# Performance work log

Hardware: AMD Instinct MI355X
Metric: run time of the kernel (lower is better)

## Reference

```python
import jax, jax.numpy as jnp
import numpy as np

D_OUT, D1, D2 = 512, 512, 512
R0, R1, R2 = 128, 128, 128
BATCH = 8192


def setup_inputs() -> dict:
    key = jax.random.key(0)
    k1, k2, k3, k4, k5, k6 = jax.random.split(key, 6)
    return {
        "X1": jax.random.normal(k1, (D1, BATCH), dtype=jnp.float32),
        "X2": jax.random.normal(k2, (D2, BATCH), dtype=jnp.float32),
        "U0": jax.random.normal(k3, (D_OUT, R0), dtype=jnp.float32) * 0.05,
        "U1": jax.random.normal(k4, (D1, R1), dtype=jnp.float32) * 0.05,
        "U2": jax.random.normal(k5, (D2, R2), dtype=jnp.float32) * 0.05,
        "G": jax.random.normal(k6, (R0, R1, R2), dtype=jnp.float32) * 0.05,
    }


def reference(X1, X2, U0, U1, U2, G):
    # Per-mode projections: UX_i = U_{i+1}^T @ X_i  -> [r_i, B]
    UX1 = U1.T @ X1  # [R1, B]
    UX2 = U2.T @ X2  # [R2, B]
    # Column-wise Khatri-Rao product of UX1, UX2 gives kron per column with
    # row index q*R2 + r (C order), which matches mode-0 unfolding of G.
    # Fused form: core = G_(0) @ khatri_rao(UX1, UX2), expressed as one einsum.
    core = jnp.einsum('pqr,qb,rb->pb', G, UX1, UX2)  # [R0, B]
    Z = U0 @ core  # [D_OUT, B]
    return Z
```

## Files before the change

kernel.cpp:

```cpp
#include <hip/hip_runtime.h>
#include <hip/hip_bf16.h>
#include <stdint.h>


typedef __attribute__((ext_vector_type(8))) short bf8;
typedef __attribute__((ext_vector_type(4))) short bf4;
typedef __attribute__((ext_vector_type(4))) float f4;

__device__ __forceinline__ unsigned short f2bf(float f){
  unsigned x = __builtin_bit_cast(unsigned, f);
  x += 0x7fffu + ((x >> 16) & 1u);
  return (unsigned short)(x >> 16);
}
__device__ __forceinline__ float bf2f(unsigned short u){
  unsigned x = ((unsigned)u) << 16;
  return __builtin_bit_cast(float, x);
}
__device__ __forceinline__ void glds16(const void* g, void* l){
  __builtin_amdgcn_global_load_lds(
      (const __attribute__((address_space(1))) void*)g,
      (__attribute__((address_space(3))) void*)l, 16, 0, 0);
}

__global__ __launch_bounds__(256) void k_cast(const float* __restrict__ G,
                                              const float* __restrict__ U0,
                                              const float* __restrict__ U1,
                                              const float* __restrict__ U2,
                                              unsigned short* __restrict__ Gbf,
                                              unsigned short* __restrict__ U0bf,
                                              unsigned short* __restrict__ U1T,
                                              unsigned short* __restrict__ U2T){
  const int blk = blockIdx.x;
  if (blk < 2112){
    const int i4 = blk * 256 + threadIdx.x;
    const int NG4 = 2097152 / 4;
    const float4* src; unsigned short* dst; int j4;
    if (i4 < NG4){ src = (const float4*)G;  dst = Gbf;  j4 = i4; }
    else         { src = (const float4*)U0; dst = U0bf; j4 = i4 - NG4; }
    float4 v = src[j4];
    ushort4 o = make_ushort4(f2bf(v.x), f2bf(v.y), f2bf(v.z), f2bf(v.w));
    ((ushort4*)dst)[j4] = o;
  } else {
    const int b2 = blk - 2112;
    const float* U = (b2 < 256) ? U1 : U2;
    unsigned short* UT = (b2 < 256) ? U1T : U2T;
    const int idx = (b2 & 255) * 256 + threadIdx.x;
    const int d = idx >> 7, q = idx & 127;
    UT[q * 512 + d] = f2bf(U[idx]);
  }
}

__global__ __launch_bounds__(256) void k_ux2(const unsigned short* __restrict__ U1T,
                                             const unsigned short* __restrict__ U2T,
                                             const float* __restrict__ X1,
                                             const float* __restrict__ X2,
                                             float* __restrict__ OUTF,
                                             unsigned short* __restrict__ OUTT){
  const bool second = (blockIdx.y != 0);
  const unsigned short* UT = second ? U2T : U1T;
  const float* X = second ? X2 : X1;
  __shared__ __align__(16) unsigned char lds[16384 + 8192];
  unsigned char* ldsA = lds;
  unsigned char* ldsB = lds + 16384;
  const int tid = threadIdx.x, lane = tid & 63, wv = tid >> 6;
  const int wr = wv >> 1, wc = wv & 1;
  const int b0 = blockIdx.x * 64;
  f4 acc[4][2] = {};

  for (int it = 0; it < 8; ++it){
    const int k0 = it * 64;
#pragma unroll
    for (int i = 0; i < 4; ++i){
      const int L = (wv * 4 + i) * 1024 + lane * 16;
      const int row = L >> 7;
      const int ss = (lane & 7) ^ (row & 7);
      glds16(UT + (size_t)row * 512 + k0 + ss * 8, ldsA + (wv * 4 + i) * 1024);
    }
#pragma unroll
    for (int c = 0; c < 2; ++c){
      const int slot = c * 4 + wv;
      const int bRow = lane;
      bf8 v;
#pragma unroll
      for (int j = 0; j < 8; ++j)
        v[j] = (short)f2bf(X[(size_t)(k0 + slot * 8 + j) * 8192 + b0 + bRow]);
      *(bf8*)(ldsB + bRow * 128 + ((slot ^ (bRow & 7)) << 4)) = v;
    }
    __syncthreads();
#pragma unroll
    for (int kc = 0; kc < 2; ++kc){
      const int g = lane >> 4;
      bf8 a[4], b[2];
#pragma unroll
      for (int mf = 0; mf < 4; ++mf){
        const int r = wr * 64 + mf * 16 + (lane & 15);
        a[mf] = *(const bf8*)(ldsA + r * 128 + (((kc * 4 + g) ^ (r & 7)) << 4));
      }
#pragma unroll
      for (int nf = 0; nf < 2; ++nf){
        const int rb = wc * 32 + nf * 16 + (lane & 15);
        b[nf] = *(const bf8*)(ldsB + rb * 128 + (((kc * 4 + g) ^ (rb & 7)) << 4));
      }
#pragma unroll
      for (int mf = 0; mf < 4; ++mf)
#pragma unroll
        for (int nf = 0; nf < 2; ++nf)
          acc[mf][nf] = __builtin_amdgcn_mfma_f32_16x16x32_bf16(a[mf], b[nf], acc[mf][nf], 0, 0, 0);
    }
    __syncthreads();
  }

  if (!second){
#pragma unroll
    for (int mf = 0; mf < 4; ++mf)
#pragma unroll
      for (int nf = 0; nf < 2; ++nf)
#pragma unroll
        for (int j = 0; j < 4; ++j){
          const int q = wr * 64 + mf * 16 + (lane >> 4) * 4 + j;
          const int b = b0 + wc * 32 + nf * 16 + (lane & 15);
          OUTF[(size_t)q * 8192 + b] = acc[mf][nf][j];
        }
  } else {
#pragma unroll
    for (int mf = 0; mf < 4; ++mf)
#pragma unroll
      for (int nf = 0; nf < 2; ++nf){
        const int rBase = wr * 64 + mf * 16 + (lane >> 4) * 4;
        const int bL = wc * 32 + nf * 16 + (lane & 15);
        bf4 p;
#pragma unroll
        for (int j = 0; j < 4; ++j) p[j] = (short)f2bf(acc[mf][nf][j]);
        *(bf4*)(lds + ((bL * 256 + rBase * 2) ^ ((bL & 7) << 4))) = p;
      }
    __syncthreads();
#pragma unroll
    for (int u = 0; u < 4; ++u){
      const int sIdx = u * 256 + tid;
      const int bL = sIdx >> 4, slot = sIdx & 15;
      bf8 v = *(const bf8*)(lds + bL * 256 + ((slot ^ (bL & 7)) << 4));
      *(bf8*)(OUTT + (size_t)(b0 + bL) * 128 + slot * 8) = v;
    }
  }
}

__global__ __launch_bounds__(512, 2) void k_core(const unsigned short* __restrict__ Gbf,
                                                 const float* __restrict__ UX1,
                                                 const unsigned short* __restrict__ UX2T,
                                                 unsigned short* __restrict__ PT){
  __shared__ __align__(16) unsigned char lds[114688];
  unsigned char* ldsX = lds + 98304;
  const int tid = threadIdx.x, lane = tid & 63, wv = tid >> 6;
  const int g = lane >> 4, l15 = lane & 15;
  const int wr = wv >> 2, wc = wv & 3;
  const int blk = blockIdx.x;
  const int split = blk & 7;
  const int b0 = (blk >> 3) * 256;
  const int q0 = split * 16;

  auto stageA = [&](int q, int buf){
#pragma unroll
    for (int rnd = 0; rnd < 4; ++rnd){
      const int off = rnd * 8192 + wv * 1024 + lane * 16;
      const int row = off >> 8;
      const int ss = ((off >> 4) & 15) ^ (row & 7);
      glds16(Gbf + (size_t)row * 16384 + (size_t)q * 128 + ss * 8,
             lds + buf * 32768 + off);
    }
  };

  bf8 Bf[4][4];
#pragma unroll
  for (int kc = 0; kc < 4; ++kc)
#pragma unroll
    for (int nf = 0; nf < 4; ++nf)
      Bf[kc][nf] = *(const bf8*)(UX2T + (size_t)(b0 + wc * 64 + nf * 16 + l15) * 128 +
                                 kc * 32 + g * 8);
#pragma unroll
  for (int rnd = 0; rnd < 2; ++rnd){
    const int off = rnd * 8192 + wv * 1024 + lane * 16;
    const int row = off >> 10;
    glds16(UX1 + (size_t)(q0 + row) * 8192 + b0 + ((off >> 2) & 255), ldsX + off);
  }
  stageA(q0 + 0, 0);
  stageA(q0 + 1, 1);

  f4 acc[4][4];
#pragma unroll
  for (int mf = 0; mf < 4; ++mf)
#pragma unroll
    for (int nf = 0; nf < 4; ++nf) acc[mf][nf] = (f4){0.f, 0.f, 0.f, 0.f};

  int cur = 0;
  for (int i = 0; i < 16; ++i){
    if (i < 15) asm volatile("s_waitcnt vmcnt(4)" ::: "memory");
    else        asm volatile("s_waitcnt vmcnt(0)" ::: "memory");
    __builtin_amdgcn_s_barrier();
    if (i < 14){
      int sbuf = cur + 2; if (sbuf >= 3) sbuf -= 3;
      stageA(q0 + i + 2, sbuf);
    }

    const unsigned char* A = lds + cur * 32768;
    float xs[4];
#pragma unroll
    for (int nf = 0; nf < 4; ++nf)
      xs[nf] = *(const float*)(ldsX + i * 1024 + (wc * 64 + nf * 16 + l15) * 4);
#pragma unroll
    for (int mf = 0; mf < 4; ++mf){
      const int row = wr * 64 + mf * 16 + l15;
      bf8 a[4];
#pragma unroll
      for (int kc = 0; kc < 4; ++kc)
        a[kc] = *(const bf8*)(A + row * 256 + ((((kc << 2) + g) ^ (row & 7)) << 4));
#pragma unroll
      for (int nf = 0; nf < 4; ++nf){
        f4 y = __builtin_amdgcn_mfma_f32_16x16x32_bf16(a[0], Bf[0][nf], (f4){0.f,0.f,0.f,0.f}, 0, 0, 0);
        y = __builtin_amdgcn_mfma_f32_16x16x32_bf16(a[1], Bf[1][nf], y, 0, 0, 0);
        y = __builtin_amdgcn_mfma_f32_16x16x32_bf16(a[2], Bf[2][nf], y, 0, 0, 0);
        y = __builtin_amdgcn_mfma_f32_16x16x32_bf16(a[3], Bf[3][nf], y, 0, 0, 0);
        acc[mf][nf] += y * xs[nf];
      }
    }
    ++cur; if (cur == 3) cur = 0;
  }

  __syncthreads();
#pragma unroll
  for (int mf = 0; mf < 4; ++mf)
#pragma unroll
    for (int nf = 0; nf < 4; ++nf){
      const int bL = wc * 64 + nf * 16 + l15;
      const int pq = wr * 16 + mf * 4 + g;
      bf4 o;
#pragma unroll
      for (int j = 0; j < 4; ++j) o[j] = (short)f2bf(acc[mf][nf][j]);
      *(bf4*)(lds + bL * 256 + ((pq ^ (bL & 7)) << 3)) = o;
    }
  __syncthreads();
#pragma unroll
  for (int rnd = 0; rnd < 8; ++rnd){
    const int idx = rnd * 512 + tid;
    const int bL = idx >> 4, s8 = idx & 15;
    bf4 lo = *(const bf4*)(lds + bL * 256 + (((s8 * 2) ^ (bL & 7)) << 3));
    bf4 hi = *(const bf4*)(lds + bL * 256 + (((s8 * 2 + 1) ^ (bL & 7)) << 3));
    bf8 o;
#pragma unroll
    for (int j = 0; j < 4; ++j){ o[j] = lo[j]; o[4 + j] = hi[j]; }
    *(bf8*)(PT + (size_t)split * 1048576 + (size_t)(b0 + bL) * 128 + s8 * 8) = o;
  }
}

__global__ __launch_bounds__(512, 1) void k_zred(const unsigned short* __restrict__ U0bf,
                                                 const unsigned short* __restrict__ PT,
                                                 float* __restrict__ Z){
  __shared__ __align__(16) unsigned char ldsB[8192];
  const int tid = threadIdx.x, lane = tid & 63, wv = tid >> 6;
  const int g = lane >> 4, l15 = lane & 15;
  const int b0 = blockIdx.x * 32;

  {
    const int b = tid >> 4, slot = tid & 15;
    float s[8] = {0.f, 0.f, 0.f, 0.f, 0.f, 0.f, 0.f, 0.f};
#pragma unroll
    for (int sp = 0; sp < 8; ++sp){
      bf8 v = *(const bf8*)(PT + ((size_t)sp * 8192 + b0 + b) * 128 + slot * 8);
#pragma unroll
      for (int j = 0; j < 8; ++j) s[j] += bf2f((unsigned short)v[j]);
    }
    bf8 o;
#pragma unroll
    for (int j = 0; j < 8; ++j) o[j] = (short)f2bf(s[j]);
    *(bf8*)(ldsB + b * 256 + ((slot ^ (b & 15)) << 4)) = o;
  }

  bf8 a[4][4];
#pragma unroll
  for (int mf = 0; mf < 4; ++mf)
#pragma unroll
    for (int kc = 0; kc < 4; ++kc)
      a[mf][kc] = *(const bf8*)(U0bf + (size_t)(wv * 64 + mf * 16 + l15) * 128 +
                                kc * 32 + g * 8);

  __syncthreads();

  f4 acc[4][2];
#pragma unroll
  for (int nf = 0; nf < 2; ++nf){
    bf8 bfr[4];
    const int row = nf * 16 + l15;
#pragma unroll
    for (int kc = 0; kc < 4; ++kc)
      bfr[kc] = *(const bf8*)(ldsB + row * 256 + ((((kc << 2) + g) ^ (row & 15)) << 4));
#pragma unroll
    for (int mf = 0; mf < 4; ++mf){
      f4 y = __builtin_amdgcn_mfma_f32_16x16x32_bf16(a[mf][0], bfr[0], (f4){0.f,0.f,0.f,0.f}, 0, 0, 0);
      y = __builtin_amdgcn_mfma_f32_16x16x32_bf16(a[mf][1], bfr[1], y, 0, 0, 0);
      y = __builtin_amdgcn_mfma_f32_16x16x32_bf16(a[mf][2], bfr[2], y, 0, 0, 0);
      y = __builtin_amdgcn_mfma_f32_16x16x32_bf16(a[mf][3], bfr[3], y, 0, 0, 0);
      acc[mf][nf] = y;
    }
  }

#pragma unroll
  for (int mf = 0; mf < 4; ++mf)
#pragma unroll
    for (int nf = 0; nf < 2; ++nf)
#pragma unroll
      for (int j = 0; j < 4; ++j){
        const int d = wv * 64 + mf * 16 + g * 4 + j;
        const int b = b0 + nf * 16 + l15;
        Z[(size_t)d * 8192 + b] = acc[mf][nf][j];
      }
}

extern "C" void kernel_launch(void* const* d_in, const int* in_sizes, int n_in,
                              void* d_out, int out_size, void* d_ws, size_t ws_size,
                              hipStream_t stream){
  const float* X1 = (const float*)d_in[0];
  const float* X2 = (const float*)d_in[1];
  const float* U0 = (const float*)d_in[2];
  const float* U1 = (const float*)d_in[3];
  const float* U2 = (const float*)d_in[4];
  const float* G  = (const float*)d_in[5];
  float* Z = (float*)d_out;

  char* ws = (char*)d_ws;
  unsigned short* Gbf   = (unsigned short*)(ws);
  unsigned short* U0bf  = (unsigned short*)(ws + 4194304);
  unsigned short* U1T   = (unsigned short*)(ws + 4325376);
  unsigned short* U2T   = (unsigned short*)(ws + 4456448);
  float*          UX1   = (float*)         (ws + 4587520);
  unsigned short* UX2T  = (unsigned short*)(ws + 8781824);
  unsigned short* PT    = (unsigned short*)(ws + 12976128);

  k_cast<<<dim3(2624), dim3(256), 0, stream>>>(G, U0, U1, U2, Gbf, U0bf, U1T, U2T);
  k_ux2 <<<dim3(128, 2), dim3(256), 0, stream>>>(U1T, U2T, X1, X2, UX1, UX2T);
  k_core<<<dim3(256), dim3(512), 0, stream>>>(Gbf, UX1, UX2T, PT);
  k_zred<<<dim3(256), dim3(512), 0, stream>>>(U0bf, PT, Z);
}
```

Baseline: 68.92 us.

## Overlap G/U0 bf16 cast with projection GEMM and widen core kernel to 1024 threads

The G and U0 casts move out of the first kernel and into extra blocks of the projection kernel, so the bandwidth-bound cast runs alongside the UX GEMMs. Only the small U1/U2 transpose-cast stays in its own launch. The core contraction kernel goes from 512 to 1024 threads per block: each wave covers 32 batch columns instead of 64, which halves per-wave register fragments and the B-operand preload. The LDS swizzle changes to XOR with the low 4 row bits and the vmcnt wait thresholds are adjusted to match. The risk is lower occupancy control, since the launch bound no longer requests 2 blocks per CU, plus more barrier cost per block.

```diff
diff --git a/kernel.cpp b/kernel.cpp
--- a/kernel.cpp
+++ b/kernel.cpp
@@ -22,17 +22,31 @@
       (__attribute__((address_space(3))) void*)l, 16, 0, 0);
 }
 
-__global__ __launch_bounds__(256) void k_cast(const float* __restrict__ G,
+__global__ __launch_bounds__(256) void k_castU(const float* __restrict__ U1,
+                                               const float* __restrict__ U2,
+                                               unsigned short* __restrict__ U1T,
+                                               unsigned short* __restrict__ U2T){
+  const int b2 = blockIdx.x;
+  const float* U = (b2 < 256) ? U1 : U2;
+  unsigned short* UT = (b2 < 256) ? U1T : U2T;
+  const int idx = (b2 & 255) * 256 + threadIdx.x;
+  const int d = idx >> 7, q = idx & 127;
+  UT[q * 512 + d] = f2bf(U[idx]);
+}
+
+__global__ __launch_bounds__(256) void k_ux2g(const unsigned short* __restrict__ U1T,
+                                              const unsigned short* __restrict__ U2T,
+                                              const float* __restrict__ X1,
+                                              const float* __restrict__ X2,
+                                              const float* __restrict__ G,
                                               const float* __restrict__ U0,
-                                              const float* __restrict__ U1,
-                                              const float* __restrict__ U2,
                                               unsigned short* __restrict__ Gbf,
                                               unsigned short* __restrict__ U0bf,
-                                              unsigned short* __restrict__ U1T,
-                                              unsigned short* __restrict__ U2T){
-  const int blk = blockIdx.x;
-  if (blk < 2112){
-    const int i4 = blk * 256 + threadIdx.x;
+                                              float* __restrict__ OUTF,
+                                              unsigned short* __restrict__ OUTT){
+  __shared__ __align__(16) unsigned char lds[16384 + 8192];
+  if (blockIdx.x >= 256){
+    const int i4 = (blockIdx.x - 256) * 256 + threadIdx.x;
     const int NG4 = 2097152 / 4;
     const float4* src; unsigned short* dst; int j4;
     if (i4 < NG4){ src = (const float4*)G;  dst = Gbf;  j4 = i4; }
@@ -40,31 +54,16 @@
     float4 v = src[j4];
     ushort4 o = make_ushort4(f2bf(v.x), f2bf(v.y), f2bf(v.z), f2bf(v.w));
     ((ushort4*)dst)[j4] = o;
-  } else {
-    const int b2 = blk - 2112;
-    const float* U = (b2 < 256) ? U1 : U2;
-    unsigned short* UT = (b2 < 256) ? U1T : U2T;
-    const int idx = (b2 & 255) * 256 + threadIdx.x;
-    const int d = idx >> 7, q = idx & 127;
-    UT[q * 512 + d] = f2bf(U[idx]);
-  }
-}
-
-__global__ __launch_bounds__(256) void k_ux2(const unsigned short* __restrict__ U1T,
-                                             const unsigned short* __restrict__ U2T,
-                                             const float* __restrict__ X1,
-                                             const float* __restrict__ X2,
-                                             float* __restrict__ OUTF,
-                                             unsigned short* __restrict__ OUTT){
-  const bool second = (blockIdx.y != 0);
+    return;
+  }
+  const bool second = (blockIdx.x >= 128);
   const unsigned short* UT = second ? U2T : U1T;
   const float* X = second ? X2 : X1;
-  __shared__ __align__(16) unsigned char lds[16384 + 8192];
   unsigned char* ldsA = lds;
   unsigned char* ldsB = lds + 16384;
   const int tid = threadIdx.x, lane = tid & 63, wv = tid >> 6;
   const int wr = wv >> 1, wc = wv & 1;
-  const int b0 = blockIdx.x * 64;
+  const int b0 = (blockIdx.x & 127) * 64;
   f4 acc[4][2] = {};
 
   for (int it = 0; it < 8; ++it){
@@ -144,15 +143,15 @@
   }
 }
 
-__global__ __launch_bounds__(512, 2) void k_core(const unsigned short* __restrict__ Gbf,
-                                                 const float* __restrict__ UX1,
-                                                 const unsigned short* __restrict__ UX2T,
-                                                 unsigned short* __restrict__ PT){
+__global__ __launch_bounds__(1024) void k_core(const unsigned short* __restrict__ Gbf,
+                                               const float* __restrict__ UX1,
+                                               const unsigned short* __restrict__ UX2T,
+                                               unsigned short* __restrict__ PT){
   __shared__ __align__(16) unsigned char lds[114688];
   unsigned char* ldsX = lds + 98304;
   const int tid = threadIdx.x, lane = tid & 63, wv = tid >> 6;
   const int g = lane >> 4, l15 = lane & 15;
-  const int wr = wv >> 2, wc = wv & 3;
+  const int wr = wv >> 3, wc = wv & 7;
   const int blk = blockIdx.x;
   const int split = blk & 7;
   const int b0 = (blk >> 3) * 256;
@@ -160,40 +159,39 @@
 
   auto stageA = [&](int q, int buf){
 #pragma unroll
-    for (int rnd = 0; rnd < 4; ++rnd){
-      const int off = rnd * 8192 + wv * 1024 + lane * 16;
+    for (int rnd = 0; rnd < 2; ++rnd){
+      const int off = rnd * 16384 + tid * 16;
       const int row = off >> 8;
-      const int ss = ((off >> 4) & 15) ^ (row & 7);
+      const int ss = ((off >> 4) & 15) ^ (row & 15);
       glds16(Gbf + (size_t)row * 16384 + (size_t)q * 128 + ss * 8,
              lds + buf * 32768 + off);
     }
   };
 
-  bf8 Bf[4][4];
+  bf8 Bf[4][2];
 #pragma unroll
   for (int kc = 0; kc < 4; ++kc)
 #pragma unroll
-    for (int nf = 0; nf < 4; ++nf)
-      Bf[kc][nf] = *(const bf8*)(UX2T + (size_t)(b0 + wc * 64 + nf * 16 + l15) * 128 +
+    for (int nf = 0; nf < 2; ++nf)
+      Bf[kc][nf] = *(const bf8*)(UX2T + (size_t)(b0 + wc * 32 + nf * 16 + l15) * 128 +
                                  kc * 32 + g * 8);
-#pragma unroll
-  for (int rnd = 0; rnd < 2; ++rnd){
-    const int off = rnd * 8192 + wv * 1024 + lane * 16;
+  {
+    const int off = tid * 16;
     const int row = off >> 10;
     glds16(UX1 + (size_t)(q0 + row) * 8192 + b0 + ((off >> 2) & 255), ldsX + off);
   }
   stageA(q0 + 0, 0);
   stageA(q0 + 1, 1);
 
-  f4 acc[4][4];
+  f4 acc[4][2];
 #pragma unroll
   for (int mf = 0; mf < 4; ++mf)
 #pragma unroll
-    for (int nf = 0; nf < 4; ++nf) acc[mf][nf] = (f4){0.f, 0.f, 0.f, 0.f};
+    for (int nf = 0; nf < 2; ++nf) acc[mf][nf] = (f4){0.f, 0.f, 0.f, 0.f};
 
   int cur = 0;
   for (int i = 0; i < 16; ++i){
-    if (i < 15) asm volatile("s_waitcnt vmcnt(4)" ::: "memory");
+    if (i < 15) asm volatile("s_waitcnt vmcnt(2)" ::: "memory");
     else        asm volatile("s_waitcnt vmcnt(0)" ::: "memory");
     __builtin_amdgcn_s_barrier();
     if (i < 14){
@@ -202,19 +200,19 @@
     }
 
     const unsigned char* A = lds + cur * 32768;
-    float xs[4];
-#pragma unroll
-    for (int nf = 0; nf < 4; ++nf)
-      xs[nf] = *(const float*)(ldsX + i * 1024 + (wc * 64 + nf * 16 + l15) * 4);
+    float xs[2];
+#pragma unroll
+    for (int nf = 0; nf < 2; ++nf)
+      xs[nf] = *(const float*)(ldsX + i * 1024 + (wc * 32 + nf * 16 + l15) * 4);
 #pragma unroll
     for (int mf = 0; mf < 4; ++mf){
       const int row = wr * 64 + mf * 16 + l15;
       bf8 a[4];
 #pragma unroll
       for (int kc = 0; kc < 4; ++kc)
-        a[kc] = *(const bf8*)(A + row * 256 + ((((kc << 2) + g) ^ (row & 7)) << 4));
-#pragma unroll
-      for (int nf = 0; nf < 4; ++nf){
+        a[kc] = *(const bf8*)(A + row * 256 + ((((kc << 2) + g) ^ l15) << 4));
+#pragma unroll
+      for (int nf = 0; nf < 2; ++nf){
         f4 y = __builtin_amdgcn_mfma_f32_16x16x32_bf16(a[0], Bf[0][nf], (f4){0.f,0.f,0.f,0.f}, 0, 0, 0);
         y = __builtin_amdgcn_mfma_f32_16x16x32_bf16(a[1], Bf[1][nf], y, 0, 0, 0);
         y = __builtin_amdgcn_mfma_f32_16x16x32_bf16(a[2], Bf[2][nf], y, 0, 0, 0);
@@ -229,8 +227,8 @@
 #pragma unroll
   for (int mf = 0; mf < 4; ++mf)
 #pragma unroll
-    for (int nf = 0; nf < 4; ++nf){
-      const int bL = wc * 64 + nf * 16 + l15;
+    for (int nf = 0; nf < 2; ++nf){
+      const int bL = wc * 32 + nf * 16 + l15;
       const int pq = wr * 16 + mf * 4 + g;
       bf4 o;
 #pragma unroll
@@ -239,8 +237,8 @@
     }
   __syncthreads();
 #pragma unroll
-  for (int rnd = 0; rnd < 8; ++rnd){
-    const int idx = rnd * 512 + tid;
+  for (int rnd = 0; rnd < 4; ++rnd){
+    const int idx = rnd * 1024 + tid;
     const int bL = idx >> 4, s8 = idx & 15;
     bf4 lo = *(const bf4*)(lds + bL * 256 + (((s8 * 2) ^ (bL & 7)) << 3));
     bf4 hi = *(const bf4*)(lds + bL * 256 + (((s8 * 2 + 1) ^ (bL & 7)) << 3));
@@ -334,8 +332,9 @@
   unsigned short* UX2T  = (unsigned short*)(ws + 8781824);
   unsigned short* PT    = (unsigned short*)(ws + 12976128);
 
-  k_cast<<<dim3(2624), dim3(256), 0, stream>>>(G, U0, U1, U2, Gbf, U0bf, U1T, U2T);
-  k_ux2 <<<dim3(128, 2), dim3(256), 0, stream>>>(U1T, U2T, X1, X2, UX1, UX2T);
-  k_core<<<dim3(256), dim3(512), 0, stream>>>(Gbf, UX1, UX2T, PT);
-  k_zred<<<dim3(256), dim3(512), 0, stream>>>(U0bf, PT, Z);
-}
+  k_castU<<<dim3(512),  dim3(256), 0, stream>>>(U1, U2, U1T, U2T);
+  k_ux2g <<<dim3(2368), dim3(256), 0, stream>>>(U1T, U2T, X1, X2, G, U0,
+                                                Gbf, U0bf, UX1, UX2T);
+  k_core <<<dim3(256), dim3(1024), 0, stream>>>(Gbf, UX1, UX2T, PT);
+  k_zred <<<dim3(256), dim3(512), 0, stream>>>(U0bf, PT, Z);
+}
```

New measurement: 69.20 us. Within noise of the previous version (+0.4%).
